# Kernel tuning notes

Measured on AMD Instinct MI355X. Metric: run time of the kernel, lower is better.

The kernel has to match this reference:

```python
import jax, jax.numpy as jnp
import numpy as np

P = 32    # cardinality (number of parallel paths)
C = 256   # block input/output channels
D = 4     # bottleneck width per path
EPS = 1e-3  # Keras BatchNormalization default epsilon


def setup_inputs() -> dict:
    key = jax.random.key(0)
    ks = jax.random.split(key, 24)
    def nrm(k, shape, s=0.05):
        return jax.random.normal(k, shape, dtype=jnp.float32) * s
    inp = {}
    inp["x"] = jax.random.normal(ks[0], (8, 56, 56, C), dtype=jnp.float32)
    # conv weights/biases, stacked over the path axis P
    inp["W1"] = nrm(ks[1], (P, C, D))          # 1x1 conv C->4
    inp["B1"] = nrm(ks[2], (P, D))
    inp["W2"] = nrm(ks[3], (P, 3, 3, D, D))    # 3x3 conv 4->4 (HWIO)
    inp["B2"] = nrm(ks[4], (P, D))
    inp["W3"] = nrm(ks[5], (P, D, C))          # 1x1 conv 4->256
    inp["B3"] = nrm(ks[6], (P, C))
    # BatchNorm (inference): gamma, beta, moving mean, moving var per stage
    inp["G1"]  = 1.0 + nrm(ks[7], (P, D));  inp["Be1"] = nrm(ks[8], (P, D))
    inp["M1"]  = nrm(ks[9], (P, D));        inp["V1"]  = 1.0 + 0.1 * jax.random.uniform(ks[10], (P, D), dtype=jnp.float32)
    inp["G2"]  = 1.0 + nrm(ks[11], (P, D)); inp["Be2"] = nrm(ks[12], (P, D))
    inp["M2"]  = nrm(ks[13], (P, D));       inp["V2"]  = 1.0 + 0.1 * jax.random.uniform(ks[14], (P, D), dtype=jnp.float32)
    inp["G3"]  = 1.0 + nrm(ks[15], (P, C)); inp["Be3"] = nrm(ks[16], (P, C))
    inp["M3"]  = nrm(ks[17], (P, C));       inp["V3"]  = 1.0 + 0.1 * jax.random.uniform(ks[18], (P, C), dtype=jnp.float32)
    return inp


def _bn(x, g, b, m, v):
    # inference batch-norm: affine over channel axis
    return g * (x - m) * jax.lax.rsqrt(v + EPS) + b


def _path(x, w1, b1, g1, be1, m1, v1, w2, b2, g2, be2, m2, v2, w3, b3, g3, be3, m3, v3):
    h = jnp.einsum('nhwc,cd->nhwd', x, w1) + b1            # 1x1 conv C->D
    h = jax.nn.relu(_bn(h, g1, be1, m1, v1))
    h = jax.lax.conv_general_dilated(
        h, w2, window_strides=(1, 1), padding='SAME',
        dimension_numbers=('NHWC', 'HWIO', 'NHWC')) + b2   # 3x3 conv D->D
    h = jax.nn.relu(_bn(h, g2, be2, m2, v2))
    h = jnp.einsum('nhwd,dc->nhwc', h, w3) + b3            # 1x1 conv D->C
    h = jax.nn.relu(_bn(h, g3, be3, m3, v3))
    return h  # Dropout(0.2) is identity at inference


def reference(x, W1, B1, G1, Be1, M1, V1, W2, B2, G2, Be2, M2, V2, W3, B3, G3, Be3, M3, V3):
    # vmap over the 32 cardinality paths; x is shared (in_axes=None)
    paths = jax.vmap(_path, in_axes=(None,) + (0,) * 18)(
        x, W1, B1, G1, Be1, M1, V1, W2, B2, G2, Be2, M2, V2, W3, B3, G3, Be3, M3, V3)
    return jax.nn.relu(paths.sum(axis=0) + x)
```

## Files before the change

kernel.cpp:

```cpp
#include <hip/hip_runtime.h>

#define BATCH 8
#define HH 56
#define WW 56
#define NPOS (BATCH*HH*WW)
#define C 256
#define P 32
#define D 4
#define J 128
#define EPS 1e-3f
#define H2S 136

typedef __attribute__((ext_vector_type(8))) short bf16x8_t;
typedef __attribute__((ext_vector_type(4))) float f32x4_t;

__device__ __forceinline__ unsigned short f2bf(float f) {
    union { float f; unsigned int i; } v; v.f = f;
    unsigned int r = v.i + 0x7fffu + ((v.i >> 16) & 1u);
    return (unsigned short)(r >> 16);
}
__device__ __forceinline__ uint2 pack4_trunc(float4 v) {
    uint2 r;
    r.x = __builtin_amdgcn_perm(__float_as_uint(v.y), __float_as_uint(v.x), 0x07060302u);
    r.y = __builtin_amdgcn_perm(__float_as_uint(v.w), __float_as_uint(v.z), 0x07060302u);
    return r;
}

__global__ __launch_bounds__(256) void fold_params(
    const float* __restrict__ W1, const float* __restrict__ B1,
    const float* __restrict__ W2, const float* __restrict__ B2,
    const float* __restrict__ W3, const float* __restrict__ B3,
    const float* __restrict__ G1, const float* __restrict__ Be1,
    const float* __restrict__ M1, const float* __restrict__ V1,
    const float* __restrict__ G2, const float* __restrict__ Be2,
    const float* __restrict__ M2, const float* __restrict__ V2,
    const float* __restrict__ G3, const float* __restrict__ Be3,
    const float* __restrict__ M3, const float* __restrict__ V3,
    unsigned short* __restrict__ W1bf, float* __restrict__ b1f,
    float* __restrict__ w2q, float* __restrict__ b2t,
    unsigned short* __restrict__ WB, unsigned short* __restrict__ zb)
{
    int idx = blockIdx.x * 256 + threadIdx.x;

    if (idx < C*J) {
        int j = idx >> 8, c = idx & 255;
        int p = j >> 2, d = j & 3;
        float s = G1[j] * rsqrtf(V1[j] + EPS);
        W1bf[idx] = f2bf(W1[(p*C + c)*D + d] * s);
        return;
    }
    idx -= C*J;
    if (idx < J) {
        float s = G1[idx] * rsqrtf(V1[idx] + EPS);
        b1f[idx] = B1[idx] * s + Be1[idx] - M1[idx] * s;
        return;
    }
    idx -= J;
    if (idx < 9*D*D*P) {
        int do_ = idx & 3, p = (idx >> 2) & 31;
        int r2 = idx >> 7, di = r2 & 3, k9 = r2 >> 2;
        int j = p*4 + do_;
        float s = G2[j] * rsqrtf(V2[j] + EPS);
        w2q[idx] = W2[((p*9 + k9)*4 + di)*4 + do_] * s;
        return;
    }
    idx -= 9*D*D*P;
    if (idx < J) {
        int do_ = idx >> 5, p = idx & 31;
        int j = p*4 + do_;
        float s = G2[j] * rsqrtf(V2[j] + EPS);
        b2t[idx] = B2[j] * s + Be2[j] - M2[j] * s;
        return;
    }
    idx -= J;
    if (idx < P*C*8) {
        int s8 = idx & 7;
        int c = (idx >> 3) & 255;
        int p = idx >> 11;
        float sc = G3[p*C + c] * rsqrtf(V3[p*C + c] + EPS);
        float v = 0.f;
        if (s8 < 4)       v = W3[(p*D + s8)*C + c] * sc;
        else if (s8 == 4) v = B3[p*C + c] * sc + Be3[p*C + c] - M3[p*C + c] * sc;
        WB[idx] = f2bf(v);
        return;
    }
    idx -= P*C*8;
    if (idx < 8) { zb[idx] = 0; return; }
}

__global__ __launch_bounds__(256) void fused_all(
    const float* __restrict__ x, const unsigned short* __restrict__ W1bf,
    const float* __restrict__ b1f, const float* __restrict__ w2q,
    const float* __restrict__ b2t, const unsigned short* __restrict__ WB,
    const unsigned short* __restrict__ zb, float* __restrict__ out)
{
    __shared__ unsigned short smem[36*256 + 36*132];
    unsigned short* xs  = smem;
    unsigned short* h1L = smem + 36*256;
    unsigned short* h2s = smem;

    const int tid = threadIdx.x;
    int bxx = blockIdx.x;
    const int xb = bxx % 14;  bxx /= 14;
    const int yb = bxx % 14;  const int b = bxx / 14;
    const int wid = tid >> 6, l = tid & 63, l15 = l & 15, quad = l >> 4;
    const int j0w = wid * 32;

#pragma unroll
    for (int it = 0; it < 5; ++it) {
        int idx = it*256 + tid;
        int pos = idx >> 5, g = idx & 31;
        if (pos < 36) {
            int hy = (pos*43) >> 8, hx = pos - hy*6;
            int gy = yb*4 + hy - 1, gx = xb*4 + hx - 1;
            uint4 st; st.x = 0u; st.y = 0u; st.z = 0u; st.w = 0u;
            if (gy >= 0 && gy < HH && gx >= 0 && gx < WW) {
                const float* xp = &x[(size_t)((b*HH + gy)*WW + gx) * C + g*8];
                float4 v0 = *(const float4*)xp;
                float4 v1 = *(const float4*)(xp + 4);
                uint2 p0 = pack4_trunc(v0), p1 = pack4_trunc(v1);
                st.x = p0.x; st.y = p0.y; st.z = p1.x; st.w = p1.y;
            }
            *(uint4*)&xs[pos*256 + ((g ^ (pos & 7)) * 8)] = st;
        }
    }
    __syncthreads();

    union bu { uint4 u; bf16x8_t v; };
#pragma unroll
    for (int jf = 0; jf < 2; ++jf) {
        bu aw[8];
        const int wrow = j0w + jf*16 + l15;
#pragma unroll
        for (int kc = 0; kc < 8; ++kc)
            aw[kc].u = *(const uint4*)&W1bf[wrow*C + kc*32 + quad*8];
#pragma unroll
        for (int mt = 0; mt < 3; ++mt) {
            const int row = mt*16 + l15;
            const int rrow = (row < 36) ? row : 0;
            int hy = (row*43) >> 8;
            int hx = row - hy*6;
            int gy = yb*4 + hy - 1, gx = xb*4 + hx - 1;
            const bool valid = (row < 36) & (gy >= 0) & (gy < HH) & (gx >= 0) & (gx < WW);
            const unsigned mask = valid ? 0xFFFFFFFFu : 0u;
            f32x4_t acc = (f32x4_t){0.f,0.f,0.f,0.f};
#pragma unroll
            for (int kc = 0; kc < 8; ++kc) {
                int g = (kc*4 + quad) ^ (rrow & 7);
                bf16x8_t bb = *(const bf16x8_t*)&xs[rrow*256 + g*8];
                acc = __builtin_amdgcn_mfma_f32_16x16x32_bf16(aw[kc].v, bb, acc, 0, 0, 0);
            }
            if (row < 36) {
                int jb = j0w + jf*16 + quad*4;
                float4 bias = *(const float4*)&b1f[jb];
                float v0 = fmaxf(acc[0] + bias.x, 0.f);
                float v1 = fmaxf(acc[1] + bias.y, 0.f);
                float v2 = fmaxf(acc[2] + bias.z, 0.f);
                float v3 = fmaxf(acc[3] + bias.w, 0.f);
                uint2 o;
                o.x = ((unsigned int)f2bf(v0) | ((unsigned int)f2bf(v1) << 16)) & mask;
                o.y = ((unsigned int)f2bf(v2) | ((unsigned int)f2bf(v3) << 16)) & mask;
                *(uint2*)&h1L[row*132 + jb] = o;
            }
        }
    }
    __syncthreads();

    const int p = tid & 31;
    const int slot = tid >> 5;
    float acc[2][4];
    {
        float b0 = b2t[p], b1 = b2t[32+p], b2 = b2t[64+p], b3 = b2t[96+p];
#pragma unroll
        for (int i = 0; i < 2; ++i) {
            acc[i][0] = b0; acc[i][1] = b1; acc[i][2] = b2; acc[i][3] = b3;
        }
    }
#pragma unroll
    for (int ky = 0; ky < 3; ++ky) {
#pragma unroll
        for (int kx = 0; kx < 3; ++kx) {
            const float* wp = &w2q[(ky*3 + kx) * 512 + p*4];
            float4 w0 = *(const float4*)&wp[0];
            float4 w1 = *(const float4*)&wp[128];
            float4 w2v = *(const float4*)&wp[256];
            float4 w3v = *(const float4*)&wp[384];
#pragma unroll
            for (int i = 0; i < 2; ++i) {
                int nl = slot + i*8;
                int hp = ((nl >> 2) + ky)*6 + (nl & 3) + kx;
                uint2 hv = *(const uint2*)&h1L[hp*132 + p*4];
                float f0 = __uint_as_float(hv.x << 16);
                float f1 = __uint_as_float(hv.x & 0xffff0000u);
                float f2 = __uint_as_float(hv.y << 16);
                float f3 = __uint_as_float(hv.y & 0xffff0000u);
                acc[i][0] = fmaf(f0, w0.x, acc[i][0]);  acc[i][1] = fmaf(f0, w0.y, acc[i][1]);
                acc[i][2] = fmaf(f0, w0.z, acc[i][2]);  acc[i][3] = fmaf(f0, w0.w, acc[i][3]);
                acc[i][0] = fmaf(f1, w1.x, acc[i][0]);  acc[i][1] = fmaf(f1, w1.y, acc[i][1]);
                acc[i][2] = fmaf(f1, w1.z, acc[i][2]);  acc[i][3] = fmaf(f1, w1.w, acc[i][3]);
                acc[i][0] = fmaf(f2, w2v.x, acc[i][0]); acc[i][1] = fmaf(f2, w2v.y, acc[i][1]);
                acc[i][2] = fmaf(f2, w2v.z, acc[i][2]); acc[i][3] = fmaf(f2, w2v.w, acc[i][3]);
                acc[i][0] = fmaf(f3, w3v.x, acc[i][0]); acc[i][1] = fmaf(f3, w3v.y, acc[i][1]);
                acc[i][2] = fmaf(f3, w3v.z, acc[i][2]); acc[i][3] = fmaf(f3, w3v.w, acc[i][3]);
            }
        }
    }
    __syncthreads();
#pragma unroll
    for (int i = 0; i < 2; ++i) {
        int nl = slot + i*8;
        uint2 o;
        o.x = (unsigned int)f2bf(fmaxf(acc[i][0], 0.f)) |
              ((unsigned int)f2bf(fmaxf(acc[i][1], 0.f)) << 16);
        o.y = (unsigned int)f2bf(fmaxf(acc[i][2], 0.f)) |
              ((unsigned int)f2bf(fmaxf(acc[i][3], 0.f)) << 16);
        *(uint2*)&h2s[nl*H2S + p*4] = o;
    }
    __syncthreads();

    const int cb = wid * 64;
    const unsigned short* wbp;
    int pstr, cstr;
    if (quad == 0) {
        wbp = &WB[((size_t)(cb + l15)) * 8];
        pstr = C * 8;
        cstr = 16 * 8;
    } else {
        wbp = zb;
        pstr = 0; cstr = 0;
    }

    const f32x4_t zero = (f32x4_t){0.f, 0.f, 0.f, 0.f};
    f32x4_t dacc[4];
#pragma unroll
    for (int ct = 0; ct < 4; ++ct) dacc[ct] = zero;
    const unsigned int one = 0x3f80u;

#pragma unroll 2
    for (int pp = 0; pp < 16; ++pp) {
        uint4 h0 = *(const uint4*)&h2s[l15*H2S + pp*8];
        union au { unsigned int u[4]; bf16x8_t v; };
        au A0, A1;
        A0.u[0] = h0.x; A0.u[1] = h0.y; A0.u[2] = one; A0.u[3] = 0u;
        A1.u[0] = h0.z; A1.u[1] = h0.w; A1.u[2] = one; A1.u[3] = 0u;
        const unsigned short* pb0 = wbp + pp*2*pstr;
        const unsigned short* pb1 = pb0 + pstr;
#pragma unroll
        for (int ct = 0; ct < 4; ++ct) {
            union bu2 { uint4 u; bf16x8_t v; } B0, B1;
            B0.u = *(const uint4*)(pb0 + ct*cstr);
            B1.u = *(const uint4*)(pb1 + ct*cstr);
            f32x4_t z0 = __builtin_amdgcn_mfma_f32_16x16x32_bf16(A0.v, B0.v, zero, 0, 0, 0);
            f32x4_t z1 = __builtin_amdgcn_mfma_f32_16x16x32_bf16(A1.v, B1.v, zero, 0, 0, 0);
#pragma unroll
            for (int r = 0; r < 4; ++r)
                dacc[ct][r] += fmaxf(z0[r], 0.f) + fmaxf(z1[r], 0.f);
        }
    }

#pragma unroll
    for (int r = 0; r < 4; ++r) {
        int nl = quad*4 + r;
        int gy = yb*4 + (nl >> 2), gx = xb*4 + (nl & 3);
        size_t n = (size_t)((b*HH + gy)*WW + gx);
        const float* xr = &x[n*C + cb + l15];
        float* orow = &out[n*C + cb + l15];
#pragma unroll
        for (int ct = 0; ct < 4; ++ct) {
            float v = dacc[ct][r] + xr[ct*16];
            orow[ct*16] = fmaxf(v, 0.f);
        }
    }
}

extern "C" void kernel_launch(void* const* d_in, const int* in_sizes, int n_in,
                              void* d_out, int out_size, void* d_ws, size_t ws_size,
                              hipStream_t stream) {
    const float* x  = (const float*)d_in[0];
    const float* W1 = (const float*)d_in[1];
    const float* B1 = (const float*)d_in[2];
    const float* W2 = (const float*)d_in[3];
    const float* B2 = (const float*)d_in[4];
    const float* W3 = (const float*)d_in[5];
    const float* B3 = (const float*)d_in[6];
    const float* G1 = (const float*)d_in[7];
    const float* Be1= (const float*)d_in[8];
    const float* M1 = (const float*)d_in[9];
    const float* V1 = (const float*)d_in[10];
    const float* G2 = (const float*)d_in[11];
    const float* Be2= (const float*)d_in[12];
    const float* M2 = (const float*)d_in[13];
    const float* V2 = (const float*)d_in[14];
    const float* G3 = (const float*)d_in[15];
    const float* Be3= (const float*)d_in[16];
    const float* M3 = (const float*)d_in[17];
    const float* V3 = (const float*)d_in[18];

    char* wsb = (char*)d_ws;
    unsigned short* W1bf = (unsigned short*)(wsb + 0);
    unsigned short* WB   = (unsigned short*)(wsb + 65536);
    float*          w2q  = (float*)(wsb + 196608);
    float*          b1f  = (float*)(wsb + 215040);
    float*          b2t  = (float*)(wsb + 215552);
    unsigned short* zb   = (unsigned short*)(wsb + 216064);

    const int fold_tasks = C*J + J + 9*D*D*P + J + P*C*8 + 8;
    fold_params<<<(fold_tasks + 255)/256, 256, 0, stream>>>(
        W1, B1, W2, B2, W3, B3, G1, Be1, M1, V1, G2, Be2, M2, V2,
        G3, Be3, M3, V3, W1bf, b1f, w2q, b2t, WB, zb);

    fused_all<<<8*14*14, 256, 0, stream>>>(x, W1bf, b1f, w2q, b2t, WB, zb,
                                           (float*)d_out);
}
```

Baseline: 188.5 us.

## Map 3x3 conv paths to producing wave, drop barriers, swizzle block order

The grouped 3x3 conv stage is remapped so each wave computes only the paths whose stage-1 outputs it wrote itself. That lets two __syncthreads be removed. h2s gets its own shared buffer instead of aliasing xs, which raises LDS use. The kernel also adds a launch-bounds occupancy hint of 4 blocks and a block-index swizzle that interleaves workgroups across XCDs. The price is more LDS per block, possible register pressure from the occupancy hint, and a changed LDS access pattern for h1L reads.

```diff
diff --git a/kernel.cpp b/kernel.cpp
--- a/kernel.cpp
+++ b/kernel.cpp
@@ -88,21 +88,21 @@
     if (idx < 8) { zb[idx] = 0; return; }
 }
 
-__global__ __launch_bounds__(256) void fused_all(
+__global__ __launch_bounds__(256, 4) void fused_all(
     const float* __restrict__ x, const unsigned short* __restrict__ W1bf,
     const float* __restrict__ b1f, const float* __restrict__ w2q,
     const float* __restrict__ b2t, const unsigned short* __restrict__ WB,
     const unsigned short* __restrict__ zb, float* __restrict__ out)
 {
-    __shared__ unsigned short smem[36*256 + 36*132];
-    unsigned short* xs  = smem;
-    unsigned short* h1L = smem + 36*256;
-    unsigned short* h2s = smem;
+    __shared__ unsigned short xs[36*256];
+    __shared__ unsigned short h1L[36*132];
+    __shared__ unsigned short h2s[16*H2S];
 
     const int tid = threadIdx.x;
-    int bxx = blockIdx.x;
-    const int xb = bxx % 14;  bxx /= 14;
-    const int yb = bxx % 14;  const int b = bxx / 14;
+    int bid = blockIdx.x;
+    int wg = (bid & 7) * 196 + (bid >> 3);
+    const int xb = wg % 14;  wg /= 14;
+    const int yb = wg % 14;  const int b = wg / 14;
     const int wid = tid >> 6, l = tid & 63, l15 = l & 15, quad = l >> 4;
     const int j0w = wid * 32;
 
@@ -164,57 +164,45 @@
             }
         }
     }
-    __syncthreads();
-
-    const int p = tid & 31;
-    const int slot = tid >> 5;
-    float acc[2][4];
-    {
-        float b0 = b2t[p], b1 = b2t[32+p], b2 = b2t[64+p], b3 = b2t[96+p];
-#pragma unroll
-        for (int i = 0; i < 2; ++i) {
-            acc[i][0] = b0; acc[i][1] = b1; acc[i][2] = b2; acc[i][3] = b3;
-        }
-    }
-#pragma unroll
-    for (int ky = 0; ky < 3; ++ky) {
-#pragma unroll
-        for (int kx = 0; kx < 3; ++kx) {
-            const float* wp = &w2q[(ky*3 + kx) * 512 + p*4];
-            float4 w0 = *(const float4*)&wp[0];
-            float4 w1 = *(const float4*)&wp[128];
-            float4 w2v = *(const float4*)&wp[256];
-            float4 w3v = *(const float4*)&wp[384];
-#pragma unroll
-            for (int i = 0; i < 2; ++i) {
-                int nl = slot + i*8;
-                int hp = ((nl >> 2) + ky)*6 + (nl & 3) + kx;
+
+    const int pos = l15;
+    const int py = pos >> 2, px = pos & 3;
+#pragma unroll
+    for (int i = 0; i < 2; ++i) {
+        const int q = (l >> 4) * 2 + i;
+        const int p = wid*8 + q;
+        float a0 = b2t[p], a1 = b2t[32+p], a2 = b2t[64+p], a3 = b2t[96+p];
+#pragma unroll
+        for (int ky = 0; ky < 3; ++ky) {
+#pragma unroll
+            for (int kx = 0; kx < 3; ++kx) {
+                const float* wp = &w2q[(ky*3 + kx) * 512 + p*4];
+                float4 w0 = *(const float4*)&wp[0];
+                float4 w1 = *(const float4*)&wp[128];
+                float4 w2v = *(const float4*)&wp[256];
+                float4 w3v = *(const float4*)&wp[384];
+                int hp = (py + ky)*6 + px + kx;
                 uint2 hv = *(const uint2*)&h1L[hp*132 + p*4];
                 float f0 = __uint_as_float(hv.x << 16);
                 float f1 = __uint_as_float(hv.x & 0xffff0000u);
                 float f2 = __uint_as_float(hv.y << 16);
                 float f3 = __uint_as_float(hv.y & 0xffff0000u);
-                acc[i][0] = fmaf(f0, w0.x, acc[i][0]);  acc[i][1] = fmaf(f0, w0.y, acc[i][1]);
-                acc[i][2] = fmaf(f0, w0.z, acc[i][2]);  acc[i][3] = fmaf(f0, w0.w, acc[i][3]);
-                acc[i][0] = fmaf(f1, w1.x, acc[i][0]);  acc[i][1] = fmaf(f1, w1.y, acc[i][1]);
-                acc[i][2] = fmaf(f1, w1.z, acc[i][2]);  acc[i][3] = fmaf(f1, w1.w, acc[i][3]);
-                acc[i][0] = fmaf(f2, w2v.x, acc[i][0]); acc[i][1] = fmaf(f2, w2v.y, acc[i][1]);
-                acc[i][2] = fmaf(f2, w2v.z, acc[i][2]); acc[i][3] = fmaf(f2, w2v.w, acc[i][3]);
-                acc[i][0] = fmaf(f3, w3v.x, acc[i][0]); acc[i][1] = fmaf(f3, w3v.y, acc[i][1]);
-                acc[i][2] = fmaf(f3, w3v.z, acc[i][2]); acc[i][3] = fmaf(f3, w3v.w, acc[i][3]);
+                a0 = fmaf(f0, w0.x, a0);  a1 = fmaf(f0, w0.y, a1);
+                a2 = fmaf(f0, w0.z, a2);  a3 = fmaf(f0, w0.w, a3);
+                a0 = fmaf(f1, w1.x, a0);  a1 = fmaf(f1, w1.y, a1);
+                a2 = fmaf(f1, w1.z, a2);  a3 = fmaf(f1, w1.w, a3);
+                a0 = fmaf(f2, w2v.x, a0); a1 = fmaf(f2, w2v.y, a1);
+                a2 = fmaf(f2, w2v.z, a2); a3 = fmaf(f2, w2v.w, a3);
+                a0 = fmaf(f3, w3v.x, a0); a1 = fmaf(f3, w3v.y, a1);
+                a2 = fmaf(f3, w3v.z, a2); a3 = fmaf(f3, w3v.w, a3);
             }
         }
-    }
-    __syncthreads();
-#pragma unroll
-    for (int i = 0; i < 2; ++i) {
-        int nl = slot + i*8;
         uint2 o;
-        o.x = (unsigned int)f2bf(fmaxf(acc[i][0], 0.f)) |
-              ((unsigned int)f2bf(fmaxf(acc[i][1], 0.f)) << 16);
-        o.y = (unsigned int)f2bf(fmaxf(acc[i][2], 0.f)) |
-              ((unsigned int)f2bf(fmaxf(acc[i][3], 0.f)) << 16);
-        *(uint2*)&h2s[nl*H2S + p*4] = o;
+        o.x = (unsigned int)f2bf(fmaxf(a0, 0.f)) |
+              ((unsigned int)f2bf(fmaxf(a1, 0.f)) << 16);
+        o.y = (unsigned int)f2bf(fmaxf(a2, 0.f)) |
+              ((unsigned int)f2bf(fmaxf(a3, 0.f)) << 16);
+        *(uint2*)&h2s[pos*H2S + p*4] = o;
     }
     __syncthreads();
 
```

Measured after the change: 175.7 us. 6.8% less time.
